# Kernel tuning notes

Measured on AMD Instinct MI355X. Metric: run time of the kernel, lower is better.

Reference implementation:

```python
import jax, jax.numpy as jnp
import numpy as np

DELTA = 1.0
EPS = 1e-8  # torch CosineSimilarity eps


def setup_inputs() -> dict:
    key = jax.random.key(0)
    k1, k2, k3, k4 = jax.random.split(key, 4)
    N1, N2, D, C = 4096, 4096, 256, 16
    return {
        "mmd1": jax.random.normal(k1, (N1, D), dtype=jnp.float32),
        "mmd2": jax.random.normal(k2, (N2, D), dtype=jnp.float32),
        "label1": jax.random.randint(k3, (N1,), 0, C, dtype=jnp.int64),
        "label2": jax.random.randint(k4, (N2,), 0, C, dtype=jnp.int64),
    }


def reference(mmd1, mmd2, label1, label2):
    # Normalize rows with torch-style eps clamp: x / max(||x||, eps)
    n1 = mmd1 / jnp.maximum(jnp.linalg.norm(mmd1, axis=1, keepdims=True), EPS)
    n2 = mmd2 / jnp.maximum(jnp.linalg.norm(mmd2, axis=1, keepdims=True), EPS)
    cos = jnp.einsum("id,jd->ij", n1, n2)  # [N1, N2] pairwise cosine
    same = label1[:, None] == label2[None, :]  # [N1, N2] bool
    per_pair = jnp.where(same, jnp.maximum(DELTA - cos, 0.0), cos)
    return jnp.mean(per_pair)
```

## Files before the change

kernel.cpp:

```cpp
#include <hip/hip_runtime.h>
#include <cstdint>

#define N1 4096
#define N2 4096
#define DD 256
#define NCLS 16
#define EPSN 1e-8f

#define MAIN_BLOCKS 128
#define ROWS_PER_BLOCK 64

#define ACC_DWORDS 8225

__global__ __launch_bounds__(256) void init_kernel(unsigned int* __restrict__ acc) {
    int idx = blockIdx.x * 256 + threadIdx.x;
    if (idx < ACC_DWORDS) acc[idx] = 0u;
}

__global__ __launch_bounds__(256) void classsum_kernel(
    const float* __restrict__ mmd1, const float* __restrict__ mmd2,
    const int* __restrict__ lab1, const int* __restrict__ lab2,
    float* __restrict__ ws_acc, float* __restrict__ out)
{
    __shared__ float part[NCLS * DD];
    __shared__ int hist[NCLS];
    __shared__ float wredS[4], wredA[4];
    __shared__ int isLast;

    float* cs1 = ws_acc;
    float* cs2 = ws_acc + NCLS * DD;
    int* cc1 = (int*)(ws_acc + 2 * NCLS * DD);
    int* cc2 = cc1 + NCLS;
    unsigned int* counter = (unsigned int*)(cc2 + NCLS);

    const int t = threadIdx.x;
    const int lane = t & 63, wid = t >> 6;
    const int side = blockIdx.x >> 6;
    const int lb = blockIdx.x & 63;

    #pragma unroll
    for (int s = t; s < NCLS * DD; s += 256) part[s] = 0.0f;
    if (t < NCLS) hist[t] = 0;
    __syncthreads();

    const float* srcbase = side ? mmd2 : mmd1;
    const int* labbase = side ? lab2 : lab1;
    const int row0 = lb * ROWS_PER_BLOCK + wid * 16;

    #pragma unroll 2
    for (int i = 0; i < 16; ++i) {
        int row = row0 + i;
        const float* src = srcbase + (size_t)row * DD;
        float x0 = src[lane];
        float x1 = src[lane + 64];
        float x2 = src[lane + 128];
        float x3 = src[lane + 192];
        float ss = x0 * x0 + x1 * x1 + x2 * x2 + x3 * x3;
        #pragma unroll
        for (int off = 32; off; off >>= 1) ss += __shfl_xor(ss, off, 64);
        float sc = 1.0f / fmaxf(sqrtf(ss), EPSN);
        int lb_ = labbase[row];
        float* prow = &part[lb_ * DD];
        atomicAdd(&prow[lane],        x0 * sc);
        atomicAdd(&prow[lane + 64],   x1 * sc);
        atomicAdd(&prow[lane + 128],  x2 * sc);
        atomicAdd(&prow[lane + 192],  x3 * sc);
        if (lane == 0) atomicAdd(&hist[lb_], 1);
    }
    __syncthreads();

    float* cs = side ? cs2 : cs1;
    #pragma unroll
    for (int s = t; s < NCLS * DD; s += 256) atomicAdd(&cs[s], part[s]);
    if (t < NCLS) atomicAdd((side ? cc2 : cc1) + t, hist[t]);

    __threadfence();
    if (t == 0) {
        unsigned int old = atomicAdd(counter, 1u);
        isLast = (old == MAIN_BLOCKS - 1) ? 1 : 0;
    }
    __syncthreads();
    if (!isLast) return;

    {
        int d = t;
        float a1 = 0.0f, a2 = 0.0f, dsame = 0.0f;
        #pragma unroll
        for (int c = 0; c < NCLS; ++c) {
            float s1 = atomicAdd(&cs1[c * DD + d], 0.0f);
            float s2 = atomicAdd(&cs2[c * DD + d], 0.0f);
            a1 += s1; a2 += s2; dsame += s1 * s2;
        }
        float dall = a1 * a2;
        #pragma unroll
        for (int off = 32; off; off >>= 1) {
            dsame += __shfl_xor(dsame, off, 64);
            dall  += __shfl_xor(dall,  off, 64);
        }
        if (lane == 0) { wredS[wid] = dsame; wredA[wid] = dall; }
        __syncthreads();
        if (t == 0) {
            float Dsame = wredS[0] + wredS[1] + wredS[2] + wredS[3];
            float Dall  = wredA[0] + wredA[1] + wredA[2] + wredA[3];
            long long scount = 0;
            for (int c = 0; c < NCLS; ++c) {
                int c1 = atomicAdd(&cc1[c], 0);
                int c2 = atomicAdd(&cc2[c], 0);
                scount += (long long)c1 * (long long)c2;
            }
            out[0] = ((float)scount + Dall - 2.0f * Dsame)
                     * (1.0f / ((float)N1 * (float)N2));
        }
    }
}

extern "C" void kernel_launch(void* const* d_in, const int* in_sizes, int n_in,
                              void* d_out, int out_size, void* d_ws, size_t ws_size,
                              hipStream_t stream) {
    const float* mmd1 = (const float*)d_in[0];
    const float* mmd2 = (const float*)d_in[1];
    const int* lab1 = (const int*)d_in[2];
    const int* lab2 = (const int*)d_in[3];

    float* ws_acc = (float*)d_ws;
    float* out = (float*)d_out;

    init_kernel<<<(ACC_DWORDS + 255) / 256, 256, 0, stream>>>((unsigned int*)ws_acc);
    classsum_kernel<<<MAIN_BLOCKS, 256, 0, stream>>>(mmd1, mmd2, lab1, lab2, ws_acc, out);
}
```

Measured before the change: 100.5 us.

## Spread class-sum over more blocks and move finalize into separate kernel

Raises the class-sum grid to 512 blocks of 512 threads, each wave handling two rows instead of sixteen, to expose more parallelism over the input rows. The last-block counter with atomic reads is replaced by a separate single-block finalize kernel launched afterwards. This cuts the serial per-block work, but it multiplies the global atomic traffic into the shared class-sum buffer and adds a kernel launch.

```diff
diff --git a/kernel.cpp b/kernel.cpp
--- a/kernel.cpp
+++ b/kernel.cpp
@@ -7,49 +7,46 @@
 #define NCLS 16
 #define EPSN 1e-8f
 
-#define MAIN_BLOCKS 128
-#define ROWS_PER_BLOCK 64
+#define CS_BLOCKS 512
+#define CS_THREADS 512
 
-#define ACC_DWORDS 8225
+#define ACC_DWORDS 8224
 
 __global__ __launch_bounds__(256) void init_kernel(unsigned int* __restrict__ acc) {
     int idx = blockIdx.x * 256 + threadIdx.x;
     if (idx < ACC_DWORDS) acc[idx] = 0u;
 }
 
-__global__ __launch_bounds__(256) void classsum_kernel(
+__global__ __launch_bounds__(CS_THREADS) void classsum_kernel(
     const float* __restrict__ mmd1, const float* __restrict__ mmd2,
     const int* __restrict__ lab1, const int* __restrict__ lab2,
-    float* __restrict__ ws_acc, float* __restrict__ out)
+    float* __restrict__ ws_acc)
 {
     __shared__ float part[NCLS * DD];
     __shared__ int hist[NCLS];
-    __shared__ float wredS[4], wredA[4];
-    __shared__ int isLast;
 
     float* cs1 = ws_acc;
     float* cs2 = ws_acc + NCLS * DD;
     int* cc1 = (int*)(ws_acc + 2 * NCLS * DD);
     int* cc2 = cc1 + NCLS;
-    unsigned int* counter = (unsigned int*)(cc2 + NCLS);
 
     const int t = threadIdx.x;
     const int lane = t & 63, wid = t >> 6;
-    const int side = blockIdx.x >> 6;
-    const int lb = blockIdx.x & 63;
+    const int side = blockIdx.x >> 8;
+    const int lb = blockIdx.x & 255;
 
     #pragma unroll
-    for (int s = t; s < NCLS * DD; s += 256) part[s] = 0.0f;
+    for (int s = t; s < NCLS * DD; s += CS_THREADS) part[s] = 0.0f;
     if (t < NCLS) hist[t] = 0;
     __syncthreads();
 
     const float* srcbase = side ? mmd2 : mmd1;
     const int* labbase = side ? lab2 : lab1;
-    const int row0 = lb * ROWS_PER_BLOCK + wid * 16;
+    const int row0 = lb * 16 + wid * 2;
 
-    #pragma unroll 2
-    for (int i = 0; i < 16; ++i) {
-        int row = row0 + i;
+    #pragma unroll
+    for (int rr = 0; rr < 2; ++rr) {
+        int row = row0 + rr;
         const float* src = srcbase + (size_t)row * DD;
         float x0 = src[lane];
         float x1 = src[lane + 64];
@@ -59,58 +56,57 @@
         #pragma unroll
         for (int off = 32; off; off >>= 1) ss += __shfl_xor(ss, off, 64);
         float sc = 1.0f / fmaxf(sqrtf(ss), EPSN);
-        int lb_ = labbase[row];
-        float* prow = &part[lb_ * DD];
+        int cls = labbase[row];
+        float* prow = &part[cls * DD];
         atomicAdd(&prow[lane],        x0 * sc);
         atomicAdd(&prow[lane + 64],   x1 * sc);
         atomicAdd(&prow[lane + 128],  x2 * sc);
         atomicAdd(&prow[lane + 192],  x3 * sc);
-        if (lane == 0) atomicAdd(&hist[lb_], 1);
+        if (lane == 0) atomicAdd(&hist[cls], 1);
     }
     __syncthreads();
 
     float* cs = side ? cs2 : cs1;
     #pragma unroll
-    for (int s = t; s < NCLS * DD; s += 256) atomicAdd(&cs[s], part[s]);
+    for (int s = t; s < NCLS * DD; s += CS_THREADS) atomicAdd(&cs[s], part[s]);
     if (t < NCLS) atomicAdd((side ? cc2 : cc1) + t, hist[t]);
+}
 
-    __threadfence();
+__global__ __launch_bounds__(256) void finalize_kernel(
+    const float* __restrict__ ws_acc, float* __restrict__ out)
+{
+    __shared__ float wredS[4], wredA[4];
+    const float* cs1 = ws_acc;
+    const float* cs2 = ws_acc + NCLS * DD;
+    const int* cc1 = (const int*)(ws_acc + 2 * NCLS * DD);
+    const int* cc2 = cc1 + NCLS;
+
+    const int t = threadIdx.x;
+    const int lane = t & 63, wid = t >> 6;
+
+    float a1 = 0.0f, a2 = 0.0f, dsame = 0.0f;
+    #pragma unroll
+    for (int c = 0; c < NCLS; ++c) {
+        float s1 = cs1[c * DD + t];
+        float s2 = cs2[c * DD + t];
+        a1 += s1; a2 += s2; dsame += s1 * s2;
+    }
+    float dall = a1 * a2;
+    #pragma unroll
+    for (int off = 32; off; off >>= 1) {
+        dsame += __shfl_xor(dsame, off, 64);
+        dall  += __shfl_xor(dall,  off, 64);
+    }
+    if (lane == 0) { wredS[wid] = dsame; wredA[wid] = dall; }
+    __syncthreads();
     if (t == 0) {
-        unsigned int old = atomicAdd(counter, 1u);
-        isLast = (old == MAIN_BLOCKS - 1) ? 1 : 0;
-    }
-    __syncthreads();
-    if (!isLast) return;
-
-    {
-        int d = t;
-        float a1 = 0.0f, a2 = 0.0f, dsame = 0.0f;
-        #pragma unroll
-        for (int c = 0; c < NCLS; ++c) {
-            float s1 = atomicAdd(&cs1[c * DD + d], 0.0f);
-            float s2 = atomicAdd(&cs2[c * DD + d], 0.0f);
-            a1 += s1; a2 += s2; dsame += s1 * s2;
-        }
-        float dall = a1 * a2;
-        #pragma unroll
-        for (int off = 32; off; off >>= 1) {
-            dsame += __shfl_xor(dsame, off, 64);
-            dall  += __shfl_xor(dall,  off, 64);
-        }
-        if (lane == 0) { wredS[wid] = dsame; wredA[wid] = dall; }
-        __syncthreads();
-        if (t == 0) {
-            float Dsame = wredS[0] + wredS[1] + wredS[2] + wredS[3];
-            float Dall  = wredA[0] + wredA[1] + wredA[2] + wredA[3];
-            long long scount = 0;
-            for (int c = 0; c < NCLS; ++c) {
-                int c1 = atomicAdd(&cc1[c], 0);
-                int c2 = atomicAdd(&cc2[c], 0);
-                scount += (long long)c1 * (long long)c2;
-            }
-            out[0] = ((float)scount + Dall - 2.0f * Dsame)
-                     * (1.0f / ((float)N1 * (float)N2));
-        }
+        float Dsame = wredS[0] + wredS[1] + wredS[2] + wredS[3];
+        float Dall  = wredA[0] + wredA[1] + wredA[2] + wredA[3];
+        float scount = 0.0f;
+        for (int c = 0; c < NCLS; ++c)
+            scount += (float)cc1[c] * (float)cc2[c];
+        out[0] = (scount + Dall - 2.0f * Dsame)
+                 * (1.0f / ((float)N1 * (float)N2));
     }
 }
 
@@ -126,5 +122,6 @@
     float* out = (float*)d_out;
 
     init_kernel<<<(ACC_DWORDS + 255) / 256, 256, 0, stream>>>((unsigned int*)ws_acc);
-    classsum_kernel<<<MAIN_BLOCKS, 256, 0, stream>>>(mmd1, mmd2, lab1, lab2, ws_acc, out);
+    classsum_kernel<<<CS_BLOCKS, CS_THREADS, 0, stream>>>(mmd1, mmd2, lab1, lab2, ws_acc);
+    finalize_kernel<<<1, 256, 0, stream>>>(ws_acc, out);
 }
```

Result: faster. 83.43 us (-17.0%).
